# Performance work log

Hardware: AMD Instinct MI355X
Metric: run time of the kernel (lower is better)

Reference implementation:

```python
import jax, jax.numpy as jnp
import numpy as np


def setup_inputs() -> dict:
    key = jax.random.key(0)
    k1, k2, k3 = jax.random.split(key, 3)
    bs, len_x, len_y, d = 8, 1024, 1024, 512
    Ex = jax.random.normal(k1, (bs, len_x, d), dtype=jnp.float32)
    Ey = jax.random.normal(k2, (bs, len_y, d), dtype=jnp.float32)
    mask_x = jnp.ones((bs, len_x, 1), dtype=bool)
    mask_y = jnp.ones((bs, len_y, 1), dtype=bool)
    W = jax.random.normal(k3, (3 * d,), dtype=jnp.float32) / np.sqrt(3 * d)
    return {"Ex": Ex, "Ey": Ey, "mask_x": mask_x, "mask_y": mask_y, "W": W}


def reference(Ex, Ey, mask_x, mask_y, W):
    # 3D branch of DualAttention (Xiong et al. 2017), dropout_rate = 0.
    bs, len_x, d = Ex.shape
    len_y = Ey.shape[1]
    w1, w2, w3 = W[:d], W[d:2 * d], W[2 * d:]
    # U[b,i,j] = [Ex_i; Ey_j; Ex_i*Ey_j] @ W  (decomposed, no 3d concat tensor)
    alpha = Ex @ w1                                   # [bs, len_x]
    beta = Ey @ w2                                    # [bs, len_y]
    cross = jnp.einsum("bid,bjd->bij", Ex, Ey * w3)   # [bs, len_x, len_y]
    U = alpha[:, :, None] + beta[None if False else slice(None), None, :] + cross
    valid = mask_x.reshape(bs, len_x, 1) & mask_y.reshape(bs, 1, len_y)
    U = jnp.where(valid, U, jnp.float32(-1e9))
    A = jax.nn.softmax(U, axis=2)                     # attend over y
    B = jnp.swapaxes(jax.nn.softmax(U, axis=1), 1, 2) # [bs, len_y, len_x]
    A_1bar = jnp.matmul(A, Ey)                        # [bs, len_x, d]
    B_1bar = jnp.matmul(B, Ex)                        # [bs, len_y, d]
    A_2bar = jnp.matmul(A, B_1bar)                    # [bs, len_x, d]
    B_2bar = jnp.matmul(B, A_1bar)                    # [bs, len_y, d]
    Gx = jnp.concatenate([Ex, A_1bar, A_2bar, Ex * A_1bar, Ex * A_2bar], axis=-1)
    Gy = jnp.concatenate([Ey, B_1bar, B_2bar, Ey * B_1bar, Ey * B_2bar], axis=-1)
    return Gx, Gy
```

## Files before the change

kernel.cpp:

```cpp
#include <hip/hip_runtime.h>
#include <stdint.h>

typedef __bf16 bf16x8 __attribute__((ext_vector_type(8)));
typedef float f32x4 __attribute__((ext_vector_type(4)));
typedef short short8v __attribute__((ext_vector_type(8)));

#define DEV static __device__ __forceinline__

DEV short f2bf(float f) {
  uint32_t u = __float_as_uint(f);
  u += 0x7fffu + ((u >> 16) & 1u);
  return (short)(u >> 16);
}

DEV float bf2f(short s) {
  return __uint_as_float(((uint32_t)(uint16_t)s) << 16);
}

DEV void llds16(const void* g, void* l) {
  __builtin_amdgcn_global_load_lds(
      (const __attribute__((address_space(1))) void*)(uintptr_t)g,
      (__attribute__((address_space(3))) void*)(uint32_t)(uintptr_t)l,
      16, 0, 0);
}

__global__ __launch_bounds__(256) void prepT_kernel(
    const float* __restrict__ Ex, const float* __restrict__ Ey,
    const float* __restrict__ W,
    float* __restrict__ alpha, float* __restrict__ beta,
    short* __restrict__ Exb, short* __restrict__ Eyw3b, short* __restrict__ Eyb,
    short* __restrict__ Exbt, short* __restrict__ Eybt,
    float* __restrict__ Gx, float* __restrict__ Gy) {
  __shared__ float red[4];
  __shared__ short lds[64 * 68];
  const int tid = threadIdx.x;
  const int bid = blockIdx.x;
  if (bid < 16384) {
    const bool isX = bid < 8192;
    const int r = isX ? bid : bid - 8192;
    const float* src = (isX ? Ex : Ey) + (size_t)r * 512;
    float2 v = *reinterpret_cast<const float2*>(src + tid * 2);
    const int wo = isX ? 0 : 512;
    float dot = v.x * W[wo + tid * 2] + v.y * W[wo + tid * 2 + 1];
    short2 bv;
    bv.x = f2bf(v.x); bv.y = f2bf(v.y);
    if (isX) {
      *reinterpret_cast<short2*>(Exb + (size_t)r * 512 + tid * 2) = bv;
    } else {
      *reinterpret_cast<short2*>(Eyb + (size_t)r * 512 + tid * 2) = bv;
      short2 wv;
      wv.x = f2bf(v.x * W[1024 + tid * 2]);
      wv.y = f2bf(v.y * W[1024 + tid * 2 + 1]);
      *reinterpret_cast<short2*>(Eyw3b + (size_t)r * 512 + tid * 2) = wv;
    }
    float* G = isX ? Gx : Gy;
    *reinterpret_cast<float2*>(G + (size_t)r * 2560 + tid * 2) = v;
    #pragma unroll
    for (int o = 32; o > 0; o >>= 1) dot += __shfl_down(dot, o);
    if ((tid & 63) == 0) red[tid >> 6] = dot;
    __syncthreads();
    if (tid == 0) (isX ? alpha : beta)[r] = red[0] + red[1] + red[2] + red[3];
  } else {
    const int t = bid - 16384;
    const int ct = t & 7, rt = (t >> 3) & 15;
    const int zz = t >> 7;
    const bool sec = zz >= 8;
    const int b = zz & 7;
    const float* src = (sec ? Ey : Ex) + (size_t)b * 1024 * 512;
    short* dst = (sec ? Eybt : Exbt) + (size_t)b * 512 * 1024;
    const int c = tid & 63, rg = tid >> 6;
    #pragma unroll
    for (int rr = 0; rr < 16; ++rr) {
      int r = rr * 4 + rg;
      float v = src[(size_t)(rt * 64 + r) * 512 + ct * 64 + c];
      lds[r * 68 + c] = f2bf(v);
    }
    __syncthreads();
    const int rl = tid & 63, cg = tid >> 6;
    #pragma unroll
    for (int cc = 0; cc < 16; ++cc) {
      int cidx = cc * 4 + cg;
      dst[(size_t)(ct * 64 + cidx) * 1024 + rt * 64 + rl] = lds[rl * 68 + cidx];
    }
  }
}

__global__ __launch_bounds__(256, 2) void gemm_u_kernel(
    const short* __restrict__ Aop, const short* __restrict__ Bop,
    const float* __restrict__ alpha, const float* __restrict__ beta,
    float* __restrict__ rowpl, float* __restrict__ colpl,
    short* __restrict__ Pe, short* __restrict__ PeT) {
  constexpr int Kdim = 512;
  constexpr int BK = 64;
  constexpr int NK = Kdim / BK;

  const int f = blockIdx.x + 8 * blockIdx.y + 64 * blockIdx.z;
  const int nf = (f & 7) * 64 + (f >> 3);
  const int bx = nf & 7, by = (nf >> 3) & 7, bz = nf >> 6;

  const int tid = threadIdx.x;
  const int lane = tid & 63;
  const int w = tid >> 6;
  const int wr = w >> 1, wc = w & 1;
  const int bt = bz;
  const int rowTile = by * 128;
  const int colTile = bx * 128;
  const size_t abase = (size_t)bt * 1024 * Kdim;
  const size_t bbase = (size_t)bt * 1024 * Kdim;

  __shared__ alignas(16) short smem[4][8192];
  __shared__ float srsum[2][128], scsum[2][128];

  auto stage = [&](int buf, int kk) {
    const int kbase = kk * BK;
    #pragma unroll
    for (int c = 0; c < 4; ++c) {
      const int byteoff = c * 4096 + w * 1024 + lane * 16;
      const int row = byteoff >> 7;
      const int col = (((byteoff & 127) ^ ((row & 7) << 4))) >> 1;
      const int uoff = (c * 4096 + w * 1024) >> 1;
      llds16(Aop + abase + (size_t)(rowTile + row) * Kdim + kbase + col,
             (void*)&smem[buf][uoff]);
      llds16(Bop + bbase + (size_t)(colTile + row) * Kdim + kbase + col,
             (void*)&smem[2 + buf][uoff]);
    }
  };

  f32x4 acc[4][4];
  #pragma unroll
  for (int m = 0; m < 4; ++m)
    #pragma unroll
    for (int n = 0; n < 4; ++n) acc[m][n] = (f32x4){0.f, 0.f, 0.f, 0.f};

  const int frow = lane & 15;
  const int fkb = (lane >> 4) * 16;
  auto sidx = [&](int r, int ko) {
    const int inrow = (ko * 64 + fkb) ^ ((r & 7) << 4);
    return r * 64 + (inrow >> 1);
  };

  stage(0, 0);
  __syncthreads();
  for (int kk = 0; kk < NK; ++kk) {
    const int cur = kk & 1;
    if (kk + 1 < NK) stage(cur ^ 1, kk + 1);
    #pragma unroll
    for (int ko = 0; ko < 2; ++ko) {
      bf16x8 af[4], bfr[4];
      #pragma unroll
      for (int m = 0; m < 4; ++m)
        af[m] = *reinterpret_cast<const bf16x8*>(
            &smem[cur][sidx(wr * 64 + m * 16 + frow, ko)]);
      #pragma unroll
      for (int n = 0; n < 4; ++n)
        bfr[n] = *reinterpret_cast<const bf16x8*>(
            &smem[2 + cur][sidx(wc * 64 + n * 16 + frow, ko)]);
      #pragma unroll
      for (int m = 0; m < 4; ++m)
        #pragma unroll
        for (int n = 0; n < 4; ++n)
          acc[m][n] = __builtin_amdgcn_mfma_f32_16x16x32_bf16(af[m], bfr[n],
                                                              acc[m][n], 0, 0, 0);
    }
    __syncthreads();
  }

  const int g4 = lane >> 4, cl = lane & 15;
  float al[16], be[4];
  #pragma unroll
  for (int m = 0; m < 4; ++m)
    #pragma unroll
    for (int j = 0; j < 4; ++j)
      al[m * 4 + j] = alpha[bt * 1024 + rowTile + wr * 64 + m * 16 + g4 * 4 + j];
  #pragma unroll
  for (int n = 0; n < 4; ++n)
    be[n] = beta[bt * 1024 + colTile + wc * 64 + n * 16 + cl];

  #pragma unroll
  for (int m = 0; m < 4; ++m)
    #pragma unroll
    for (int n = 0; n < 4; ++n)
      #pragma unroll
      for (int j = 0; j < 4; ++j)
        acc[m][n][j] = __expf(acc[m][n][j] + al[m * 4 + j] + be[n]);

  short* ats = &smem[0][0];
  #pragma unroll
  for (int m = 0; m < 4; ++m)
    #pragma unroll
    for (int j = 0; j < 4; ++j) {
      const int r = wr * 64 + m * 16 + g4 * 4 + j;
      float s = 0.f;
      #pragma unroll
      for (int n = 0; n < 4; ++n) {
        const float e = acc[m][n][j];
        s += e;
        ats[r * 136 + wc * 64 + n * 16 + cl] = f2bf(e);
      }
      s += __shfl_xor(s, 1);
      s += __shfl_xor(s, 2);
      s += __shfl_xor(s, 4);
      s += __shfl_xor(s, 8);
      if (cl == 0) srsum[wc][r] = s;
    }
  #pragma unroll
  for (int n = 0; n < 4; ++n) {
    const int c = wc * 64 + n * 16 + cl;
    float s = 0.f;
    #pragma unroll
    for (int m = 0; m < 4; ++m)
      #pragma unroll
      for (int j = 0; j < 4; ++j) s += acc[m][n][j];
    s += __shfl_xor(s, 16);
    s += __shfl_xor(s, 32);
    if (g4 == 0) scsum[wr][c] = s;
  }
  __syncthreads();
  if (tid < 128) {
    const size_t o = (size_t)bx * 8192 + bt * 1024 + rowTile + tid;
    rowpl[o] = srsum[0][tid] + srsum[1][tid];
  } else {
    const int t = tid - 128;
    const size_t o = (size_t)by * 8192 + bt * 1024 + colTile + t;
    colpl[o] = scsum[0][t] + scsum[1][t];
  }
  {
    const int r = tid >> 1, half = tid & 1;
    const size_t gb = ((size_t)bt * 1024 + rowTile + r) * 1024 + colTile + half * 64;
    #pragma unroll
    for (int k = 0; k < 8; ++k)
      *reinterpret_cast<short8v*>(&Pe[gb + k * 8]) =
          *reinterpret_cast<const short8v*>(&ats[r * 136 + half * 64 + k * 8]);
  }
  __syncthreads();
  #pragma unroll
  for (int m = 0; m < 4; ++m) {
    const int r0 = wr * 64 + m * 16 + g4 * 4;
    #pragma unroll
    for (int n = 0; n < 4; ++n) {
      const int c = wc * 64 + n * 16 + cl;
      short4 tb;
      #pragma unroll
      for (int j = 0; j < 4; ++j) ((short*)&tb)[j] = f2bf(acc[m][n][j]);
      *reinterpret_cast<short4*>(&ats[c * 132 + r0]) = tb;
    }
  }
  __syncthreads();
  {
    const int c = tid >> 1, half = tid & 1;
    const size_t gb = ((size_t)bt * 1024 + colTile + c) * 1024 + rowTile + half * 64;
    #pragma unroll
    for (int k = 0; k < 8; ++k)
      *reinterpret_cast<short8v*>(&PeT[gb + k * 8]) =
          *reinterpret_cast<const short8v*>(&ats[c * 132 + half * 64 + k * 8]);
  }
}

__global__ __launch_bounds__(256) void combine_kernel(
    const float* __restrict__ rowpl, const float* __restrict__ colpl,
    float* __restrict__ arow, float* __restrict__ bcol) {
  const int g = blockIdx.x * 256 + threadIdx.x;
  float L = 0.f, Lc = 0.f;
  #pragma unroll
  for (int p = 0; p < 8; ++p) {
    L += rowpl[p * 8192 + g];
    Lc += colpl[p * 8192 + g];
  }
  arow[g] = 1.0f / L;
  bcol[g] = 1.0f / Lc;
}

template <int MODE>
__global__ __launch_bounds__(256, 2) void gemm_dual(
    const short* __restrict__ A1, const short* __restrict__ B1,
    const short* __restrict__ E1, float* __restrict__ G1, short* __restrict__ T1,
    const float* __restrict__ S1,
    const short* __restrict__ A2, const short* __restrict__ B2,
    const short* __restrict__ E2, float* __restrict__ G2, short* __restrict__ T2,
    const float* __restrict__ S2) {
  constexpr int Kdim = 1024;
  constexpr int BK = 64;
  constexpr int NK = Kdim / BK;

  const int f = blockIdx.x + 4 * blockIdx.y + 32 * blockIdx.z;
  const int nf = (f & 7) * 64 + (f >> 3);
  const int bx = nf & 3, by = (nf >> 2) & 7, bz = nf >> 5;

  const bool sec = bz >= 8;
  const int bt = bz & 7;
  const short* Aop = sec ? A2 : A1;
  const short* Bop = sec ? B2 : B1;
  const short* Emat = sec ? E2 : E1;
  float* G = sec ? G2 : G1;
  short* T = sec ? T2 : T1;
  const float* Svec = sec ? S2 : S1;

  const int tid = threadIdx.x;
  const int lane = tid & 63;
  const int w = tid >> 6;
  const int wr = w >> 1, wc = w & 1;
  const int rowTile = by * 128;
  const int colTile = bx * 128;
  const size_t abase = (size_t)bt * 1024 * Kdim;
  const size_t bbase = (size_t)bt * 512 * Kdim;

  __shared__ alignas(16) short smem[4][8192];

  auto stage = [&](int buf, int kk) {
    const int kbase = kk * BK;
    #pragma unroll
    for (int c = 0; c < 4; ++c) {
      const int byteoff = c * 4096 + w * 1024 + lane * 16;
      const int row = byteoff >> 7;
      const int col = (((byteoff & 127) ^ ((row & 7) << 4))) >> 1;
      const int uoff = (c * 4096 + w * 1024) >> 1;
      llds16(Aop + abase + (size_t)(rowTile + row) * Kdim + kbase + col,
             (void*)&smem[buf][uoff]);
      llds16(Bop + bbase + (size_t)(colTile + row) * Kdim + kbase + col,
             (void*)&smem[2 + buf][uoff]);
    }
  };

  f32x4 acc[4][4];
  #pragma unroll
  for (int m = 0; m < 4; ++m)
    #pragma unroll
    for (int n = 0; n < 4; ++n) acc[m][n] = (f32x4){0.f, 0.f, 0.f, 0.f};

  const int frow = lane & 15;
  const int fkb = (lane >> 4) * 16;
  auto sidx = [&](int r, int ko) {
    const int inrow = (ko * 64 + fkb) ^ ((r & 7) << 4);
    return r * 64 + (inrow >> 1);
  };

  stage(0, 0);
  __syncthreads();
  for (int kk = 0; kk < NK; ++kk) {
    const int cur = kk & 1;
    if (kk + 1 < NK) stage(cur ^ 1, kk + 1);
    #pragma unroll
    for (int ko = 0; ko < 2; ++ko) {
      bf16x8 af[4], bfr[4];
      #pragma unroll
      for (int m = 0; m < 4; ++m)
        af[m] = *reinterpret_cast<const bf16x8*>(
            &smem[cur][sidx(wr * 64 + m * 16 + frow, ko)]);
      #pragma unroll
      for (int n = 0; n < 4; ++n)
        bfr[n] = *reinterpret_cast<const bf16x8*>(
            &smem[2 + cur][sidx(wc * 64 + n * 16 + frow, ko)]);
      #pragma unroll
      for (int m = 0; m < 4; ++m)
        #pragma unroll
        for (int n = 0; n < 4; ++n)
          acc[m][n] = __builtin_amdgcn_mfma_f32_16x16x32_bf16(af[m], bfr[n],
                                                              acc[m][n], 0, 0, 0);
    }
    __syncthreads();
  }

  const int g4 = lane >> 4, cl = lane & 15;
  float sc[16];
  #pragma unroll
  for (int m = 0; m < 4; ++m)
    #pragma unroll
    for (int j = 0; j < 4; ++j)
      sc[m * 4 + j] = Svec[bt * 1024 + rowTile + wr * 64 + m * 16 + g4 * 4 + j];

  short* tls = &smem[0][0];
  #pragma unroll
  for (int m = 0; m < 4; ++m) {
    #pragma unroll
    for (int n = 0; n < 4; ++n) {
      const int rl0 = wr * 64 + m * 16 + g4 * 4;
      const int cloc = wc * 64 + n * 16 + cl;
      const int row0 = rowTile + rl0;
      const int col = colTile + cloc;
      short4 tb;
      #pragma unroll
      for (int j = 0; j < 4; ++j) {
        const int row = row0 + j;
        const float val = acc[m][n][j] * sc[m * 4 + j];
        const size_t e = ((size_t)bt * 1024 + row) * 512 + col;
        const float ex = bf2f(Emat[e]);
        const size_t g = ((size_t)bt * 1024 + row) * 2560;
        if constexpr (MODE == 1) {
          G[g + 512 + col] = val;
          G[g + 1536 + col] = val * ex;
          ((short*)&tb)[j] = f2bf(val);
        } else {
          G[g + 1024 + col] = val;
          G[g + 2048 + col] = val * ex;
        }
      }
      if constexpr (MODE == 1)
        *reinterpret_cast<short4*>(&tls[cloc * 136 + rl0]) = tb;
    }
  }
  if constexpr (MODE == 1) {
    __syncthreads();
    const int r2 = tid >> 1, half = tid & 1;
    const size_t tb = ((size_t)bt * 512 + colTile + r2) * 1024 + rowTile + half * 64;
    #pragma unroll
    for (int k = 0; k < 8; ++k)
      *reinterpret_cast<short8v*>(&T[tb + k * 8]) =
          *reinterpret_cast<const short8v*>(&tls[r2 * 136 + half * 64 + k * 8]);
  }
}

extern "C" void kernel_launch(void* const* d_in, const int* in_sizes, int n_in,
                              void* d_out, int out_size, void* d_ws, size_t ws_size,
                              hipStream_t stream) {
  const float* Ex = (const float*)d_in[0];
  const float* Ey = (const float*)d_in[1];
  const float* W = (const float*)d_in[4];

  float* Gx = (float*)d_out;
  float* Gy = Gx + (size_t)8 * 1024 * 2560;

  char* wsP = (char*)d_ws;
  auto cv = [&](size_t bytes) {
    char* p = wsP;
    wsP += (bytes + 255) & ~(size_t)255;
    return (void*)p;
  };
  const size_t BL = (size_t)8 * 1024;
  float* alpha   = (float*)cv(BL * 4);
  float* beta    = (float*)cv(BL * 4);
  float* arow    = (float*)cv(BL * 4);
  float* bcol    = (float*)cv(BL * 4);
  float* rowpl   = (float*)cv(8 * BL * 4);
  float* colpl   = (float*)cv(8 * BL * 4);
  short* Exb     = (short*)cv(BL * 512 * 2);
  short* Eyw3b   = (short*)cv(BL * 512 * 2);
  short* Eyb     = (short*)cv(BL * 512 * 2);
  short* Exbt    = (short*)cv(BL * 512 * 2);
  short* Eybt    = (short*)cv(BL * 512 * 2);
  short* A1t     = (short*)cv(BL * 512 * 2);
  short* B1t     = (short*)cv(BL * 512 * 2);
  short* Pe      = (short*)cv(BL * 1024 * 2);
  short* PeT     = (short*)cv(BL * 1024 * 2);

  prepT_kernel<<<18432, 256, 0, stream>>>(Ex, Ey, W, alpha, beta, Exb, Eyw3b, Eyb,
                                          Exbt, Eybt, Gx, Gy);
  gemm_u_kernel<<<dim3(8, 8, 8), 256, 0, stream>>>(
      Exb, Eyw3b, alpha, beta, rowpl, colpl, Pe, PeT);
  combine_kernel<<<32, 256, 0, stream>>>(rowpl, colpl, arow, bcol);
  gemm_dual<1><<<dim3(4, 8, 16), 256, 0, stream>>>(
      Pe, Eybt, Exb, Gx, A1t, arow, PeT, Exbt, Eyb, Gy, B1t, bcol);
  gemm_dual<2><<<dim3(4, 8, 16), 256, 0, stream>>>(
      Pe, B1t, Exb, Gx, nullptr, arow, PeT, A1t, Eyb, Gy, nullptr, bcol);
}
```

Before: 118.5 us.

## Pipeline GEMM K-loop two stages ahead with explicit waitcnt and barriers

Replaces the double-buffered K loop in both GEMM kernels with a deeper schedule. The loop prefetches two K-tiles up front and loads all LDS fragments for a tile into registers first. It then barriers and issues the next global-to-LDS load into the freed buffer before running the MFMAs, waiting on vmcnt with explicit s_waitcnt. The goal is to hide global load latency behind MFMA work and drop one sync per iteration, at the cost of more fragment registers and extra barriers added before the epilogue reuses shared memory.

```diff
diff --git a/kernel.cpp b/kernel.cpp
--- a/kernel.cpp
+++ b/kernel.cpp
@@ -85,6 +85,45 @@
   }
 }
 
+#define KLOOP_PIPE(NKv)                                                        \
+  stage(0, 0);                                                                 \
+  stage(1, 1);                                                                 \
+  asm volatile("s_waitcnt vmcnt(8)" ::: "memory");                             \
+  __builtin_amdgcn_s_barrier();                                                \
+  for (int kk = 0; kk < NKv; ++kk) {                                           \
+    const int cur = kk & 1;                                                    \
+    bf16x8 af[2][4], bfr[2][4];                                                \
+    _Pragma("unroll")                                                          \
+    for (int ko = 0; ko < 2; ++ko) {                                           \
+      _Pragma("unroll")                                                        \
+      for (int m = 0; m < 4; ++m)                                              \
+        af[ko][m] = *reinterpret_cast<const bf16x8*>(                          \
+            &smem[cur][sidx(wr * 64 + m * 16 + frow, ko)]);                    \
+      _Pragma("unroll")                                                        \
+      for (int n = 0; n < 4; ++n)                                              \
+        bfr[ko][n] = *reinterpret_cast<const bf16x8*>(                         \
+            &smem[2 + cur][sidx(wc * 64 + n * 16 + frow, ko)]);                \
+    }                                                                          \
+    asm volatile("s_waitcnt lgkmcnt(0)" ::: "memory");                         \
+    __builtin_amdgcn_sched_barrier(0);                                         \
+    __builtin_amdgcn_s_barrier();                                              \
+    if (kk + 2 < NKv) stage(cur, kk + 2);                                      \
+    _Pragma("unroll")                                                          \
+    for (int ko = 0; ko < 2; ++ko)                                             \
+      _Pragma("unroll")                                                        \
+      for (int m = 0; m < 4; ++m)                                              \
+        _Pragma("unroll")                                                      \
+        for (int n = 0; n < 4; ++n)                                            \
+          acc[m][n] = __builtin_amdgcn_mfma_f32_16x16x32_bf16(                 \
+              af[ko][m], bfr[ko][n], acc[m][n], 0, 0, 0);                      \
+    if (kk + 2 < NKv) {                                                        \
+      asm volatile("s_waitcnt vmcnt(8)" ::: "memory");                         \
+    } else if (kk + 1 < NKv) {                                                 \
+      asm volatile("s_waitcnt vmcnt(0)" ::: "memory");                         \
+    }                                                                          \
+    __builtin_amdgcn_s_barrier();                                              \
+  }
+
 __global__ __launch_bounds__(256, 2) void gemm_u_kernel(
     const short* __restrict__ Aop, const short* __restrict__ Bop,
     const float* __restrict__ alpha, const float* __restrict__ beta,
@@ -139,31 +178,7 @@
     return r * 64 + (inrow >> 1);
   };
 
-  stage(0, 0);
-  __syncthreads();
-  for (int kk = 0; kk < NK; ++kk) {
-    const int cur = kk & 1;
-    if (kk + 1 < NK) stage(cur ^ 1, kk + 1);
-    #pragma unroll
-    for (int ko = 0; ko < 2; ++ko) {
-      bf16x8 af[4], bfr[4];
-      #pragma unroll
-      for (int m = 0; m < 4; ++m)
-        af[m] = *reinterpret_cast<const bf16x8*>(
-            &smem[cur][sidx(wr * 64 + m * 16 + frow, ko)]);
-      #pragma unroll
-      for (int n = 0; n < 4; ++n)
-        bfr[n] = *reinterpret_cast<const bf16x8*>(
-            &smem[2 + cur][sidx(wc * 64 + n * 16 + frow, ko)]);
-      #pragma unroll
-      for (int m = 0; m < 4; ++m)
-        #pragma unroll
-        for (int n = 0; n < 4; ++n)
-          acc[m][n] = __builtin_amdgcn_mfma_f32_16x16x32_bf16(af[m], bfr[n],
-                                                              acc[m][n], 0, 0, 0);
-    }
-    __syncthreads();
-  }
+  KLOOP_PIPE(NK)
 
   const int g4 = lane >> 4, cl = lane & 15;
   float al[16], be[4];
@@ -184,6 +199,7 @@
       for (int j = 0; j < 4; ++j)
         acc[m][n][j] = __expf(acc[m][n][j] + al[m * 4 + j] + be[n]);
 
+  __syncthreads();
   short* ats = &smem[0][0];
   #pragma unroll
   for (int m = 0; m < 4; ++m)
@@ -334,31 +350,7 @@
     return r * 64 + (inrow >> 1);
   };
 
-  stage(0, 0);
-  __syncthreads();
-  for (int kk = 0; kk < NK; ++kk) {
-    const int cur = kk & 1;
-    if (kk + 1 < NK) stage(cur ^ 1, kk + 1);
-    #pragma unroll
-    for (int ko = 0; ko < 2; ++ko) {
-      bf16x8 af[4], bfr[4];
-      #pragma unroll
-      for (int m = 0; m < 4; ++m)
-        af[m] = *reinterpret_cast<const bf16x8*>(
-            &smem[cur][sidx(wr * 64 + m * 16 + frow, ko)]);
-      #pragma unroll
-      for (int n = 0; n < 4; ++n)
-        bfr[n] = *reinterpret_cast<const bf16x8*>(
-            &smem[2 + cur][sidx(wc * 64 + n * 16 + frow, ko)]);
-      #pragma unroll
-      for (int m = 0; m < 4; ++m)
-        #pragma unroll
-        for (int n = 0; n < 4; ++n)
-          acc[m][n] = __builtin_amdgcn_mfma_f32_16x16x32_bf16(af[m], bfr[n],
-                                                              acc[m][n], 0, 0, 0);
-    }
-    __syncthreads();
-  }
+  KLOOP_PIPE(NK)
 
   const int g4 = lane >> 4, cl = lane & 15;
   float sc[16];
@@ -368,6 +360,7 @@
     for (int j = 0; j < 4; ++j)
       sc[m * 4 + j] = Svec[bt * 1024 + rowTile + wr * 64 + m * 16 + g4 * 4 + j];
 
+  if constexpr (MODE == 1) __syncthreads();
   short* tls = &smem[0][0];
   #pragma unroll
   for (int m = 0; m < 4; ++m) {
```

Result: faster. 115.0 us (-2.9%).
